# Kernel tuning notes

Measured on AMD Instinct MI355X. Metric: run time of the kernel, lower is better.

Reference implementation:

```python
import jax, jax.numpy as jnp
import numpy as np

B, L, D, H = 4, 1024, 1024, 16
HS = D // H
BLOCK = 1024
EPS = 1e-5


def setup_inputs() -> dict:
    key = jax.random.key(0)
    ks = jax.random.split(key, 12)
    s = 0.02
    return {
        "x": jax.random.normal(ks[0], (B, L, D), jnp.float32),
        "ln1_w": jnp.ones((D,), jnp.float32),
        "ln1_b": jnp.zeros((D,), jnp.float32),
        "Wqkv": jax.random.normal(ks[1], (D, 3 * D), jnp.float32) * s,
        "bqkv": jnp.zeros((3 * D,), jnp.float32),
        "Wproj": jax.random.normal(ks[2], (D, D), jnp.float32) * s,
        "bproj": jnp.zeros((D,), jnp.float32),
        "Er": jax.random.normal(ks[3], (BLOCK, HS), jnp.float32) * s,
        "ln2_w": jnp.ones((D,), jnp.float32),
        "ln2_b": jnp.zeros((D,), jnp.float32),
        "Wfc": jax.random.normal(ks[4], (D, 4 * D), jnp.float32) * s,
        "bfc": jnp.zeros((4 * D,), jnp.float32),
        "Wfc2": jax.random.normal(ks[5], (4 * D, D), jnp.float32) * s,
        "bfc2": jnp.zeros((D,), jnp.float32),
    }


def _layernorm(x, w, b):
    mu = jnp.mean(x, axis=-1, keepdims=True)
    var = jnp.mean(jnp.square(x - mu), axis=-1, keepdims=True)
    return (x - mu) * jax.lax.rsqrt(var + EPS) * w + b


def _skew(QEr):
    # Music-Transformer skew: pad one zero column on the left of last dim,
    # reshape (B,H,L,L+1) -> (B,H,L+1,L), drop first row.
    b, h, l, _ = QEr.shape
    padded = jnp.pad(QEr, ((0, 0), (0, 0), (0, 0), (1, 0)))
    return padded.reshape(b, h, l + 1, l)[:, :, 1:, :]


def _block(x, ln1_w, ln1_b, Wqkv, bqkv, Wproj, bproj, Er,
           ln2_w, ln2_b, Wfc, bfc, Wfc2, bfc2):
    b, l, d = x.shape
    # --- attention on ln_1(x) ---
    h = _layernorm(x, ln1_w, ln1_b)
    qkv = h @ Wqkv + bqkv                      # (B, L, 3D)
    q, k, v = jnp.split(qkv, 3, axis=-1)
    q = q.reshape(b, l, H, HS).transpose(0, 2, 1, 3)  # (B,H,L,hs)
    k = k.reshape(b, l, H, HS).transpose(0, 2, 1, 3)
    v = v.reshape(b, l, H, HS).transpose(0, 2, 1, 3)

    start = BLOCK - l
    Er_t = Er[start:, :].T                     # (hs, L)
    QEr = jnp.einsum('bhld,dm->bhlm', q, Er_t)  # (B,H,L,L)
    Srel = _skew(QEr)

    QKt = jnp.einsum('bhld,bhmd->bhlm', q, k)  # (B,H,L,L)
    scale = 1.0 / jnp.sqrt(jnp.asarray(HS, x.dtype))
    att = (QKt + Srel) * scale
    causal = jnp.tril(jnp.ones((l, l), bool))
    att = jnp.where(causal, att, jnp.asarray(-jnp.inf, att.dtype))
    att = jax.nn.softmax(att, axis=-1)
    y = jnp.einsum('bhlm,bhmd->bhld', att, v)  # (B,H,L,hs)
    y = y.transpose(0, 2, 1, 3).reshape(b, l, d)
    a = y @ Wproj + bproj

    x = x + a
    # --- MLP on ln_2(x) ---
    h2 = _layernorm(x, ln2_w, ln2_b)
    m = jax.nn.gelu(h2 @ Wfc + bfc, approximate=False) @ Wfc2 + bfc2
    return x + m


def reference(x, ln1_w, ln1_b, Wqkv, bqkv, Wproj, bproj, Er,
              ln2_w, ln2_b, Wfc, bfc, Wfc2, bfc2):
    return _block(x, ln1_w, ln1_b, Wqkv, bqkv, Wproj, bproj, Er,
                  ln2_w, ln2_b, Wfc, bfc, Wfc2, bfc2)
```

## Files before the change

### kernel.cpp

```cpp
#include <hip/hip_runtime.h>
#include <hip/hip_bf16.h>
#include <math.h>

typedef __attribute__((ext_vector_type(8))) __bf16 bf16x8;
typedef __attribute__((ext_vector_type(4))) float f32x4;

#define LL 1024
#define DD 1024
#define HH 16

#define GLOAD16(g, l)                                              \
  __builtin_amdgcn_global_load_lds(                                \
      (const __attribute__((address_space(1))) void*)(g),          \
      (__attribute__((address_space(3))) void*)(l), 16, 0, 0)

#define FENCE asm volatile("" ::: "memory")
#define SCHEDB __builtin_amdgcn_sched_barrier(0)
#define BARRIER do { FENCE; __builtin_amdgcn_s_barrier(); FENCE; } while (0)

__global__ __launch_bounds__(256) void prep_weights(const float* __restrict__ Wqkv,
                                                    const float* __restrict__ Wproj,
                                                    const float* __restrict__ Wfc,
                                                    const float* __restrict__ Wfc2,
                                                    const float* __restrict__ Er,
                                                    __hip_bfloat16* __restrict__ Wqkvt,
                                                    __hip_bfloat16* __restrict__ Wprojt,
                                                    __hip_bfloat16* __restrict__ Wfct,
                                                    __hip_bfloat16* __restrict__ Wfc2t,
                                                    __hip_bfloat16* __restrict__ Erb) {
  int bid = blockIdx.x;
  int tx = threadIdx.x;
  if (bid >= 12288) {
    int i = (bid - 12288) * 256 + tx;
    float4 v = *(const float4*)&Er[(size_t)i * 4];
    __hip_bfloat16 o[4];
    o[0] = __float2bfloat16(v.x); o[1] = __float2bfloat16(v.y);
    o[2] = __float2bfloat16(v.z); o[3] = __float2bfloat16(v.w);
    *(uint2*)&Erb[(size_t)i * 4] = *(const uint2*)o;
    return;
  }
  const float* W; __hip_bfloat16* Wt; int R, C, local;
  if (bid < 3072)      { W = Wqkv;  Wt = Wqkvt;  R = 1024; C = 3072; local = bid; }
  else if (bid < 4096) { W = Wproj; Wt = Wprojt; R = 1024; C = 1024; local = bid - 3072; }
  else if (bid < 8192) { W = Wfc;   Wt = Wfct;   R = 1024; C = 4096; local = bid - 4096; }
  else                 { W = Wfc2;  Wt = Wfc2t;  R = 4096; C = 1024; local = bid - 8192; }
  int nbx = C / 32;
  int r0 = (local / nbx) * 32, c0 = (local % nbx) * 32;
  __shared__ float tile[32][33];
  int r = tx >> 3, c4 = (tx & 7) * 4;
  float4 v = *(const float4*)&W[(size_t)(r0 + r) * C + c0 + c4];
  tile[r][c4 + 0] = v.x; tile[r][c4 + 1] = v.y;
  tile[r][c4 + 2] = v.z; tile[r][c4 + 3] = v.w;
  __syncthreads();
  int c = tx >> 3, r4 = (tx & 7) * 4;
  __hip_bfloat16 o[4];
#pragma unroll
  for (int j = 0; j < 4; ++j) o[j] = __float2bfloat16(tile[r4 + j][c]);
  *(uint2*)&Wt[(size_t)(c0 + c) * R + r0 + r4] = *(const uint2*)o;
}

__global__ __launch_bounds__(256) void ln_kernel(const float* __restrict__ X,
                                                 const float* __restrict__ w,
                                                 const float* __restrict__ b,
                                                 __hip_bfloat16* __restrict__ out) {
  int row = blockIdx.x;
  int tid = threadIdx.x;
  const float* xr = X + (size_t)row * DD;
  float4 v = *(const float4*)&xr[tid * 4];
  float s = v.x + v.y + v.z + v.w;
  float s2 = v.x * v.x + v.y * v.y + v.z * v.z + v.w * v.w;
#pragma unroll
  for (int m = 1; m < 64; m <<= 1) {
    s += __shfl_xor(s, m);
    s2 += __shfl_xor(s2, m);
  }
  __shared__ float ps[4], ps2[4];
  int wv_ = tid >> 6, lane = tid & 63;
  if (lane == 0) { ps[wv_] = s; ps2[wv_] = s2; }
  __syncthreads();
  float ts = ps[0] + ps[1] + ps[2] + ps[3];
  float ts2 = ps2[0] + ps2[1] + ps2[2] + ps2[3];
  float mu = ts * (1.0f / DD);
  float var = ts2 * (1.0f / DD) - mu * mu;
  float rs = rsqrtf(var + 1e-5f);
  float4 wv = *(const float4*)&w[tid * 4];
  float4 bv = *(const float4*)&b[tid * 4];
  __hip_bfloat16 o[4];
  o[0] = __float2bfloat16((v.x - mu) * rs * wv.x + bv.x);
  o[1] = __float2bfloat16((v.y - mu) * rs * wv.y + bv.y);
  o[2] = __float2bfloat16((v.z - mu) * rs * wv.z + bv.z);
  o[3] = __float2bfloat16((v.w - mu) * rs * wv.w + bv.w);
  *(uint2*)&out[(size_t)row * DD + tid * 4] = *(const uint2*)o;
}

template <int EPI>
__global__ __launch_bounds__(256, 4) void gemm128sq(const __hip_bfloat16* __restrict__ A,
                                                    const __hip_bfloat16* __restrict__ Bt,
                                                    const float* __restrict__ bias,
                                                    const float* __restrict__ resid,
                                                    void* __restrict__ Cout,
                                                    int M, int N, int K) {
  __shared__ __hip_bfloat16 Ab[2][128][32];
  __shared__ __hip_bfloat16 Bb[2][128][32];
  const int tid = threadIdx.x, lane = tid & 63, w = tid >> 6;
  const int wm = w >> 1, wn = w & 1;

  int nbx = gridDim.x, nwg = nbx * gridDim.y;
  int orig = blockIdx.y * nbx + blockIdx.x;
  int cpx = nwg >> 3;
  int wgid = (orig & 7) * cpx + (orig >> 3);
  int bm0 = (wgid / nbx) * 128, bn0 = (wgid % nbx) * 128;

  const int fr = lane & 15, kq = lane >> 4;
  const int sg = ((lane & 3) ^ ((lane >> 3) & 3)) * 8;
  const int srw = lane >> 2;

  auto stageA = [&](int c, int g, int k0) {
    int u = w * 2 + g;
    const __hip_bfloat16* src = A + (size_t)(bm0 + u * 16 + srw) * K + k0 + sg;
    GLOAD16(src, (char*)Ab + c * 8192 + u * 1024);
  };
  auto stageB = [&](int c, int g, int k0) {
    int u = w * 2 + g;
    const __hip_bfloat16* src = Bt + (size_t)(bn0 + u * 16 + srw) * K + k0 + sg;
    GLOAD16(src, (char*)Bb + c * 8192 + u * 1024);
  };
  const int swz = ((kq ^ ((fr >> 1) & 3)) << 4);
  auto ldA = [&](int c, int r) -> bf16x8 {
    return *(const bf16x8*)((const char*)Ab + c * 8192 + r * 64 + swz);
  };
  auto ldB = [&](int c, int r) -> bf16x8 {
    return *(const bf16x8*)((const char*)Bb + c * 8192 + r * 64 + swz);
  };

  f32x4 acc[4][4] = {};
  bf16x8 a[4], b[4];

  const int nt = K >> 5;
  stageA(0, 0, 0);  stageA(0, 1, 0);  stageB(0, 0, 0);  stageB(0, 1, 0);
  stageA(1, 0, 32); stageA(1, 1, 32); stageB(1, 0, 32); stageB(1, 1, 32);
  asm volatile("s_waitcnt vmcnt(4)" ::: "memory");
  BARRIER;

  for (int t = 0; t < nt; ++t) {
    const int cur = t & 1;
#pragma unroll
    for (int mf = 0; mf < 4; ++mf) a[mf] = ldA(cur, wm * 64 + mf * 16 + fr);
#pragma unroll
    for (int nf = 0; nf < 4; ++nf) b[nf] = ldB(cur, wn * 64 + nf * 16 + fr);
    __builtin_amdgcn_s_setprio(1);
#pragma unroll
    for (int mf = 0; mf < 4; ++mf)
#pragma unroll
      for (int nf = 0; nf < 4; ++nf)
        acc[mf][nf] = __builtin_amdgcn_mfma_f32_16x16x32_bf16(a[mf], b[nf], acc[mf][nf], 0, 0, 0);
    __builtin_amdgcn_s_setprio(0);
    BARRIER;
    if (t + 2 < nt) {
      int kn = (t + 2) * 32;
      stageA(cur, 0, kn); stageA(cur, 1, kn); stageB(cur, 0, kn); stageB(cur, 1, kn);
      asm volatile("s_waitcnt vmcnt(4)" ::: "memory");
    } else if (t + 1 < nt) {
      asm volatile("s_waitcnt vmcnt(0)" ::: "memory");
    }
    BARRIER;
  }

#pragma unroll
  for (int nf = 0; nf < 4; ++nf) {
    int col = bn0 + wn * 64 + nf * 16 + fr;
    float bsv = bias[col];
#pragma unroll
    for (int mf = 0; mf < 4; ++mf) {
      int rowb = bm0 + wm * 64 + mf * 16 + kq * 4;
#pragma unroll
      for (int j = 0; j < 4; ++j) {
        int row = rowb + j;
        float v = acc[mf][nf][j] + bsv;
        if (EPI == 1) v = 0.5f * v * (1.0f + erff(v * 0.7071067811865476f));
        if (EPI == 2) {
          ((float*)Cout)[(size_t)row * N + col] = v + resid[(size_t)row * N + col];
        } else {
          ((__hip_bfloat16*)Cout)[(size_t)row * N + col] = __float2bfloat16(v);
        }
      }
    }
  }
}

template <int EPI>
__global__ __launch_bounds__(512, 4) void gemm128x64w8(const __hip_bfloat16* __restrict__ A,
                                                       const __hip_bfloat16* __restrict__ Bt,
                                                       const float* __restrict__ bias,
                                                       const float* __restrict__ resid,
                                                       void* __restrict__ Cout,
                                                       int M, int N, int K) {
  __shared__ __hip_bfloat16 Ab[3][128][64];
  __shared__ __hip_bfloat16 Bb[3][64][64];
  const int tid = threadIdx.x, lane = tid & 63, w = tid >> 6;
  const int wm = w >> 1, wn = w & 1;

  int nbx = gridDim.x, nwg = nbx * gridDim.y;
  int orig = blockIdx.y * nbx + blockIdx.x;
  int cpx = nwg >> 3;
  int wgid = (orig & 7) * cpx + (orig >> 3);
  int bm0 = (wgid / nbx) * 128, bn0 = (wgid % nbx) * 64;

  const int fr = lane & 15, kq = lane >> 4;
  const int srw = lane >> 3;
  const int sg = ((lane & 7) ^ (lane >> 3)) * 8;

  auto stageA = [&](int c, int j, int k0) {
    int u = 2 * w + j;
    const __hip_bfloat16* src = A + (size_t)(bm0 + u * 8 + srw) * K + k0 + sg;
    GLOAD16(src, (char*)Ab + c * 16384 + u * 1024);
  };
  auto stageB = [&](int c, int k0) {
    const __hip_bfloat16* src = Bt + (size_t)(bn0 + w * 8 + srw) * K + k0 + sg;
    GLOAD16(src, (char*)Bb + c * 8192 + w * 1024);
  };
  auto ldA = [&](int c, int r, int ks) -> bf16x8 {
    int byte = r * 128 + ((ks * 64 + kq * 16) ^ ((r & 7) << 4));
    return *(const bf16x8*)((const char*)Ab + c * 16384 + byte);
  };
  auto ldB = [&](int c, int r, int ks) -> bf16x8 {
    int byte = r * 128 + ((ks * 64 + kq * 16) ^ ((r & 7) << 4));
    return *(const bf16x8*)((const char*)Bb + c * 8192 + byte);
  };

  f32x4 acc[2][2] = {};
  bf16x8 a[2][2], b[2][2];

  const int nt = K >> 6;
#pragma unroll
  for (int tt = 0; tt < 2; ++tt) {
    stageA(tt, 0, tt * 64); stageA(tt, 1, tt * 64); stageB(tt, tt * 64);
  }
  asm volatile("s_waitcnt vmcnt(3)" ::: "memory");
  BARRIER;

  int cur = 0, nxt = 2;
  for (int t = 0; t < nt; ++t) {
#pragma unroll
    for (int mf = 0; mf < 2; ++mf)
#pragma unroll
      for (int ks = 0; ks < 2; ++ks)
        a[mf][ks] = ldA(cur, wm * 32 + mf * 16 + fr, ks);
#pragma unroll
    for (int nf = 0; nf < 2; ++nf)
#pragma unroll
      for (int ks = 0; ks < 2; ++ks)
        b[nf][ks] = ldB(cur, wn * 32 + nf * 16 + fr, ks);
    if (t + 2 < nt) {
      stageA(nxt, 0, (t + 2) * 64); stageA(nxt, 1, (t + 2) * 64); stageB(nxt, (t + 2) * 64);
    }
    __builtin_amdgcn_s_setprio(1);
#pragma unroll
    for (int mf = 0; mf < 2; ++mf)
#pragma unroll
      for (int nf = 0; nf < 2; ++nf)
#pragma unroll
        for (int ks = 0; ks < 2; ++ks)
          acc[mf][nf] = __builtin_amdgcn_mfma_f32_16x16x32_bf16(
              a[mf][ks], b[nf][ks], acc[mf][nf], 0, 0, 0);
    __builtin_amdgcn_s_setprio(0);
    if (t <= nt - 3)      { asm volatile("s_waitcnt vmcnt(3)" ::: "memory"); }
    else if (t == nt - 2) { asm volatile("s_waitcnt vmcnt(0)" ::: "memory"); }
    BARRIER;
    cur = (cur == 2) ? 0 : cur + 1;
    nxt = (nxt == 2) ? 0 : nxt + 1;
  }

#pragma unroll
  for (int nf = 0; nf < 2; ++nf) {
    int col = bn0 + wn * 32 + nf * 16 + fr;
    float bsv = bias[col];
#pragma unroll
    for (int mf = 0; mf < 2; ++mf) {
      int rowb = bm0 + wm * 32 + mf * 16 + kq * 4;
#pragma unroll
      for (int j = 0; j < 4; ++j) {
        int row = rowb + j;
        float v = acc[mf][nf][j] + bsv;
        if (EPI == 1) v = 0.5f * v * (1.0f + erff(v * 0.7071067811865476f));
        if (EPI == 2) {
          ((float*)Cout)[(size_t)row * N + col] = v + resid[(size_t)row * N + col];
        } else {
          ((__hip_bfloat16*)Cout)[(size_t)row * N + col] = __float2bfloat16(v);
        }
      }
    }
  }
}

__global__ __launch_bounds__(256) void attn_mfma(const __hip_bfloat16* __restrict__ qkv,
                                                 const __hip_bfloat16* __restrict__ Erb,
                                                 __hip_bfloat16* __restrict__ Y) {
  __shared__ __hip_bfloat16 k_s[64][72];
  __shared__ __hip_bfloat16 er_s[64][72];
  __shared__ __hip_bfloat16 p_s[4][16][72];
  __shared__ __hip_bfloat16 g_s[4][16][132];
  __shared__ __hip_bfloat16 vt_s[64 * 64];

  int bid = blockIdx.x;
  int qi = 15 - (bid >> 6);
  int head = bid & 63;
  int h = head & 15, b = head >> 4;
  int l0 = qi * 64;
  int tid = threadIdx.x, lane = tid & 63, w = tid >> 6;
  const int fr = lane & 15, kq = lane >> 4;

  const __hip_bfloat16* base = qkv + (size_t)b * (LL * 3072) + h * 64;

  bf16x8 qf[2];
  {
    const __hip_bfloat16* q0 = base + (size_t)(l0 + 16 * w + fr) * 3072 + kq * 8;
    qf[0] = *(const bf16x8*)q0;
    qf[1] = *(const bf16x8*)(q0 + 32);
  }

  const int ksr = tid >> 2, ksd = (tid & 3) * 16;
  const __hip_bfloat16* ksrc = base + 1024 + (size_t)ksr * 3072 + ksd;
  const int vc = (tid >> 3) * 2, vd0 = (tid & 7) * 8;
  const __hip_bfloat16* vsrc = base + 2048 + (size_t)vc * 3072 + vd0;
  const int err = tid >> 2, erc = (tid & 3) * 16;

  uint4 kst0, kst1, vst0, vst1;
  uint4 ers0, ers1;
  uint4 ec10, ec11;

  {
    kst0 = *(const uint4*)ksrc; kst1 = *(const uint4*)(ksrc + 8);
    vst0 = *(const uint4*)vsrc; vst1 = *(const uint4*)(vsrc + 3072);
    int m0 = min(max(960 - l0 + err, 0), 1023);
    const __hip_bfloat16* ep0 = Erb + (size_t)m0 * 64 + erc;
    ers0 = *(const uint4*)ep0; ers1 = *(const uint4*)(ep0 + 8);
    if (qi > 0) {
      int m1 = min(max(960 - l0 + 64 + err, 0), 1023);
      const __hip_bfloat16* ep1 = Erb + (size_t)m1 * 64 + erc;
      ec10 = *(const uint4*)ep1; ec11 = *(const uint4*)(ep1 + 8);
    }
  }

  f32x4 oacc[4] = {};
  float m_run[4], s_run[4];
#pragma unroll
  for (int j = 0; j < 4; ++j) { m_run[j] = -1e30f; s_run[j] = 0.f; }

  auto gchunk = [&](int hf) {
#pragma unroll
    for (int g = 0; g < 4; ++g) {
      int cc = 16 * g + fr, kc = kq * 8;
      bf16x8 e0 = *(const bf16x8*)&er_s[cc][kc];
      bf16x8 e1 = *(const bf16x8*)&er_s[cc][kc + 32];
      f32x4 gacc = {};
      gacc = __builtin_amdgcn_mfma_f32_16x16x32_bf16(qf[0], e0, gacc, 0, 0, 0);
      gacc = __builtin_amdgcn_mfma_f32_16x16x32_bf16(qf[1], e1, gacc, 0, 0, 0);
#pragma unroll
      for (int j = 0; j < 4; ++j)
        g_s[w][kq * 4 + j][hf * 64 + 16 * g + fr] = __float2bfloat16(gacc[j]);
    }
  };

  for (int t = 0; t <= qi; ++t) {
    __syncthreads();
    *(uint4*)&k_s[ksr][ksd] = kst0;
    *(uint4*)&k_s[ksr][ksd + 8] = kst1;
    {
      const uint16_t* h0 = (const uint16_t*)&vst0;
      const uint16_t* h1 = (const uint16_t*)&vst1;
#pragma unroll
      for (int j = 0; j < 8; ++j) {
        int d = vd0 + j;
        uint32_t pk = (uint32_t)h0[j] | ((uint32_t)h1[j] << 16);
        uint32_t byte = ((uint32_t)d << 7) + 2u * (uint32_t)vc;
        byte ^= (uint32_t)(((d & 7) ^ (d >> 3)) << 4);
        *(uint32_t*)((char*)vt_s + byte) = pk;
      }
    }
    if (t == 0 || t < qi) {
      *(uint4*)&er_s[err][erc]     = ers0;
      *(uint4*)&er_s[err][erc + 8] = ers1;
    }
    __syncthreads();
    if (t < qi) {
      int c0n = (t + 1) * 64;
      const __hip_bfloat16* kp = ksrc + (size_t)c0n * 3072;
      kst0 = *(const uint4*)kp; kst1 = *(const uint4*)(kp + 8);
      const __hip_bfloat16* vp = vsrc + (size_t)c0n * 3072;
      vst0 = *(const uint4*)vp; vst1 = *(const uint4*)(vp + 3072);
      if (t + 1 < qi) {
        int m = min(960 - l0 + (t + 2) * 64 + err, 1023);
        const __hip_bfloat16* ep = Erb + (size_t)m * 64 + erc;
        ers0 = *(const uint4*)ep; ers1 = *(const uint4*)(ep + 8);
      }
    }
    SCHEDB;

    f32x4 sacc[4] = {};
#pragma unroll
    for (int f = 0; f < 4; ++f) {
      int cc = 16 * f + fr, kc = kq * 8;
      bf16x8 k0 = *(const bf16x8*)&k_s[cc][kc];
      bf16x8 k1 = *(const bf16x8*)&k_s[cc][kc + 32];
      sacc[f] = __builtin_amdgcn_mfma_f32_16x16x32_bf16(qf[0], k0, sacc[f], 0, 0, 0);
      sacc[f] = __builtin_amdgcn_mfma_f32_16x16x32_bf16(qf[1], k1, sacc[f], 0, 0, 0);
    }
    if (t == 0) {
      gchunk(0);
      if (qi > 0) {
        __syncthreads();
        *(uint4*)&er_s[err][erc]     = ec10;
        *(uint4*)&er_s[err][erc + 8] = ec11;
        __syncthreads();
        gchunk(1);
      }
    } else if (t < qi) {
      gchunk((t + 1) & 1);
    }

    float sv[4][4];
#pragma unroll
    for (int f = 0; f < 4; ++f) {
#pragma unroll
      for (int j = 0; j < 4; ++j) {
        int r = kq * 4 + j;
        int c = 16 * f + fr;
        int jj = c - (16 * w + r) + 63;
        float g = __bfloat162float(g_s[w][r][(t * 64 + jj) & 127]);
        float val = (sacc[f][j] + g) * 0.125f;
        if (t == qi && c > 16 * w + r) val = -1e30f;
        sv[f][j] = val;
      }
    }
    float tm[4];
#pragma unroll
    for (int j = 0; j < 4; ++j) {
      float m_ = fmaxf(fmaxf(sv[0][j], sv[1][j]), fmaxf(sv[2][j], sv[3][j]));
      m_ = fmaxf(m_, __shfl_xor(m_, 1));
      m_ = fmaxf(m_, __shfl_xor(m_, 2));
      m_ = fmaxf(m_, __shfl_xor(m_, 4));
      m_ = fmaxf(m_, __shfl_xor(m_, 8));
      tm[j] = m_;
    }
    bool need = (tm[0] > m_run[0] + 8.f) || (tm[1] > m_run[1] + 8.f) ||
                (tm[2] > m_run[2] + 8.f) || (tm[3] > m_run[3] + 8.f);
    float alpha[4];
    if (need) {
#pragma unroll
      for (int j = 0; j < 4; ++j) {
        float nm = fmaxf(m_run[j], tm[j]);
        alpha[j] = __expf(m_run[j] - nm);
        m_run[j] = nm;
      }
    }
#pragma unroll
    for (int f = 0; f < 4; ++f)
#pragma unroll
      for (int j = 0; j < 4; ++j)
        sv[f][j] = __expf(sv[f][j] - m_run[j]);
#pragma unroll
    for (int j = 0; j < 4; ++j) {
      float ps = sv[0][j] + sv[1][j] + sv[2][j] + sv[3][j];
      ps += __shfl_xor(ps, 1); ps += __shfl_xor(ps, 2);
      ps += __shfl_xor(ps, 4); ps += __shfl_xor(ps, 8);
      s_run[j] = (need ? s_run[j] * alpha[j] : s_run[j]) + ps;
    }
    if (need) {
#pragma unroll
      for (int f = 0; f < 4; ++f)
#pragma unroll
        for (int j = 0; j < 4; ++j)
          oacc[f][j] *= alpha[j];
    }
#pragma unroll
    for (int f = 0; f < 4; ++f)
#pragma unroll
      for (int j = 0; j < 4; ++j)
        p_s[w][kq * 4 + j][16 * f + fr] = __float2bfloat16(sv[f][j]);
#pragma unroll
    for (int kk = 0; kk < 2; ++kk) {
      bf16x8 pf = *(const bf16x8*)&p_s[w][fr][kq * 8 + 32 * kk];
#pragma unroll
      for (int f = 0; f < 4; ++f) {
        int d = 16 * f + fr;
        int cc = kq * 8 + 32 * kk;
        uint32_t byte = ((uint32_t)d << 7) + 2u * (uint32_t)cc;
        byte ^= (uint32_t)(((d & 7) ^ (d >> 3)) << 4);
        bf16x8 vf = *(const bf16x8*)((char*)vt_s + byte);
        oacc[f] = __builtin_amdgcn_mfma_f32_16x16x32_bf16(pf, vf, oacc[f], 0, 0, 0);
      }
    }
  }

#pragma unroll
  for (int f = 0; f < 4; ++f)
#pragma unroll
    for (int j = 0; j < 4; ++j) {
      int r = 16 * w + kq * 4 + j;
      int d = 16 * f + fr;
      float o = oacc[f][j] / s_run[j];
      Y[(size_t)(b * LL + l0 + r) * DD + h * 64 + d] = __float2bfloat16(o);
    }
}

extern "C" void kernel_launch(void* const* d_in, const int* in_sizes, int n_in,
                              void* d_out, int out_size, void* d_ws, size_t ws_size,
                              hipStream_t stream) {
  (void)in_sizes; (void)n_in; (void)out_size; (void)ws_size;
  const float* x     = (const float*)d_in[0];
  const float* ln1w  = (const float*)d_in[1];
  const float* ln1b  = (const float*)d_in[2];
  const float* Wqkv  = (const float*)d_in[3];
  const float* bqkv  = (const float*)d_in[4];
  const float* Wproj = (const float*)d_in[5];
  const float* bproj = (const float*)d_in[6];
  const float* Er    = (const float*)d_in[7];
  const float* ln2w  = (const float*)d_in[8];
  const float* ln2b  = (const float*)d_in[9];
  const float* Wfc   = (const float*)d_in[10];
  const float* bfc   = (const float*)d_in[11];
  const float* Wfc2  = (const float*)d_in[12];
  const float* bfc2  = (const float*)d_in[13];
  float* out = (float*)d_out;

  char* ws = (char*)d_ws;
  const size_t MB = 1ull << 20;
  __hip_bfloat16* h1    = (__hip_bfloat16*)(ws + 0);
  __hip_bfloat16* qkvb  = (__hip_bfloat16*)(ws + 8 * MB);
  __hip_bfloat16* mbuf  = (__hip_bfloat16*)(ws + 0);
  __hip_bfloat16* yb    = (__hip_bfloat16*)(ws + 32 * MB);
  __hip_bfloat16* h2    = (__hip_bfloat16*)(ws + 32 * MB);
  float*          x2    = (float*)(ws + 40 * MB);
  __hip_bfloat16* Wqkvt = (__hip_bfloat16*)(ws + 56 * MB);
  __hip_bfloat16* Erb   = (__hip_bfloat16*)(ws + 62 * MB);
  __hip_bfloat16* Wprojt= (__hip_bfloat16*)(ws + 63 * MB);
  __hip_bfloat16* Wfct  = (__hip_bfloat16*)(ws + 66 * MB);
  __hip_bfloat16* Wfc2t = (__hip_bfloat16*)(ws + 75 * MB);

  dim3 blk(256);

  prep_weights<<<dim3(12352), blk, 0, stream>>>(Wqkv, Wproj, Wfc, Wfc2, Er,
                                                Wqkvt, Wprojt, Wfct, Wfc2t, Erb);

  ln_kernel<<<4096, blk, 0, stream>>>(x, ln1w, ln1b, h1);

  gemm128sq<0><<<dim3(3072 / 128, 4096 / 128), blk, 0, stream>>>(
      h1, Wqkvt, bqkv, nullptr, qkvb, 4096, 3072, 1024);

  attn_mfma<<<dim3(1024), blk, 0, stream>>>(qkvb, Erb, yb);

  gemm128x64w8<2><<<dim3(1024 / 64, 4096 / 128), dim3(512), 0, stream>>>(
      yb, Wprojt, bproj, x, x2, 4096, 1024, 1024);

  ln_kernel<<<4096, blk, 0, stream>>>(x2, ln2w, ln2b, h2);

  gemm128sq<1><<<dim3(4096 / 128, 4096 / 128), blk, 0, stream>>>(
      h2, Wfct, bfc, nullptr, mbuf, 4096, 4096, 1024);

  gemm128x64w8<2><<<dim3(1024 / 64, 4096 / 128), dim3(512), 0, stream>>>(
      mbuf, Wfc2t, bfc2, x2, out, 4096, 1024, 4096);
}
```

Before: 223.9 us.

## Replace LDS-staged GEMM with direct global-to-register double-buffered loads

The 128x128 GEMM used for QKV and FC1 no longer stages A and B tiles through shared memory. Each wave now loads its MFMA fragments straight from global memory into registers, double-buffered across k-steps, and all barriers are gone. The workgroup-to-tile remapping is also changed to a new XCD-aware grouping. The aim is to remove LDS traffic and sync overhead, at the cost of redundant global/L2 reads across waves and higher register pressure (launch bounds lowered to 3).

```diff
diff --git a/kernel.cpp b/kernel.cpp
--- a/kernel.cpp
+++ b/kernel.cpp
@@ -94,60 +94,38 @@
 }
 
 template <int EPI>
-__global__ __launch_bounds__(256, 4) void gemm128sq(const __hip_bfloat16* __restrict__ A,
-                                                    const __hip_bfloat16* __restrict__ Bt,
-                                                    const float* __restrict__ bias,
-                                                    const float* __restrict__ resid,
-                                                    void* __restrict__ Cout,
-                                                    int M, int N, int K) {
-  __shared__ __hip_bfloat16 Ab[2][128][32];
-  __shared__ __hip_bfloat16 Bb[2][128][32];
+__global__ __launch_bounds__(256, 3) void gemm128d(const __hip_bfloat16* __restrict__ A,
+                                                   const __hip_bfloat16* __restrict__ Bt,
+                                                   const float* __restrict__ bias,
+                                                   const float* __restrict__ resid,
+                                                   void* __restrict__ Cout,
+                                                   int M, int N, int K) {
   const int tid = threadIdx.x, lane = tid & 63, w = tid >> 6;
   const int wm = w >> 1, wn = w & 1;
 
   int nbx = gridDim.x, nwg = nbx * gridDim.y;
   int orig = blockIdx.y * nbx + blockIdx.x;
-  int cpx = nwg >> 3;
-  int wgid = (orig & 7) * cpx + (orig >> 3);
-  int bm0 = (wgid / nbx) * 128, bn0 = (wgid % nbx) * 128;
+  int cpx = nwg >> 3, CC = cpx >> 3;
+  int x = orig & 7, kk = orig >> 3;
+  int row = ((x >> 1) << 3) + (kk & 7);
+  int col = (x & 1) * CC + (kk >> 3);
+  int bm0 = row * 128, bn0 = col * 128;
 
   const int fr = lane & 15, kq = lane >> 4;
-  const int sg = ((lane & 3) ^ ((lane >> 3) & 3)) * 8;
-  const int srw = lane >> 2;
-
-  auto stageA = [&](int c, int g, int k0) {
-    int u = w * 2 + g;
-    const __hip_bfloat16* src = A + (size_t)(bm0 + u * 16 + srw) * K + k0 + sg;
-    GLOAD16(src, (char*)Ab + c * 8192 + u * 1024);
-  };
-  auto stageB = [&](int c, int g, int k0) {
-    int u = w * 2 + g;
-    const __hip_bfloat16* src = Bt + (size_t)(bn0 + u * 16 + srw) * K + k0 + sg;
-    GLOAD16(src, (char*)Bb + c * 8192 + u * 1024);
-  };
-  const int swz = ((kq ^ ((fr >> 1) & 3)) << 4);
-  auto ldA = [&](int c, int r) -> bf16x8 {
-    return *(const bf16x8*)((const char*)Ab + c * 8192 + r * 64 + swz);
-  };
-  auto ldB = [&](int c, int r) -> bf16x8 {
-    return *(const bf16x8*)((const char*)Bb + c * 8192 + r * 64 + swz);
-  };
+
+  const __hip_bfloat16* ap[4];
+  const __hip_bfloat16* bp[4];
+#pragma unroll
+  for (int mf = 0; mf < 4; ++mf)
+    ap[mf] = A + (size_t)(bm0 + wm * 64 + mf * 16 + fr) * K + kq * 8;
+#pragma unroll
+  for (int nf = 0; nf < 4; ++nf)
+    bp[nf] = Bt + (size_t)(bn0 + wn * 64 + nf * 16 + fr) * K + kq * 8;
 
   f32x4 acc[4][4] = {};
-  bf16x8 a[4], b[4];
-
-  const int nt = K >> 5;
-  stageA(0, 0, 0);  stageA(0, 1, 0);  stageB(0, 0, 0);  stageB(0, 1, 0);
-  stageA(1, 0, 32); stageA(1, 1, 32); stageB(1, 0, 32); stageB(1, 1, 32);
-  asm volatile("s_waitcnt vmcnt(4)" ::: "memory");
-  BARRIER;
-
-  for (int t = 0; t < nt; ++t) {
-    const int cur = t & 1;
-#pragma unroll
-    for (int mf = 0; mf < 4; ++mf) a[mf] = ldA(cur, wm * 64 + mf * 16 + fr);
-#pragma unroll
-    for (int nf = 0; nf < 4; ++nf) b[nf] = ldB(cur, wn * 64 + nf * 16 + fr);
+  bf16x8 a0[4], b0[4], a1[4], b1[4];
+
+  auto mmq = [&](bf16x8* a, bf16x8* b) {
     __builtin_amdgcn_s_setprio(1);
 #pragma unroll
     for (int mf = 0; mf < 4; ++mf)
@@ -155,33 +133,45 @@
       for (int nf = 0; nf < 4; ++nf)
         acc[mf][nf] = __builtin_amdgcn_mfma_f32_16x16x32_bf16(a[mf], b[nf], acc[mf][nf], 0, 0, 0);
     __builtin_amdgcn_s_setprio(0);
-    BARRIER;
+  };
+
+  const int nt = K >> 5;
+#pragma unroll
+  for (int mf = 0; mf < 4; ++mf) a0[mf] = *(const bf16x8*)ap[mf];
+#pragma unroll
+  for (int nf = 0; nf < 4; ++nf) b0[nf] = *(const bf16x8*)bp[nf];
+
+  for (int t = 0; t < nt; t += 2) {
+#pragma unroll
+    for (int mf = 0; mf < 4; ++mf) a1[mf] = *(const bf16x8*)(ap[mf] + (t + 1) * 32);
+#pragma unroll
+    for (int nf = 0; nf < 4; ++nf) b1[nf] = *(const bf16x8*)(bp[nf] + (t + 1) * 32);
+    mmq(a0, b0);
     if (t + 2 < nt) {
-      int kn = (t + 2) * 32;
-      stageA(cur, 0, kn); stageA(cur, 1, kn); stageB(cur, 0, kn); stageB(cur, 1, kn);
-      asm volatile("s_waitcnt vmcnt(4)" ::: "memory");
-    } else if (t + 1 < nt) {
-      asm volatile("s_waitcnt vmcnt(0)" ::: "memory");
-    }
-    BARRIER;
+#pragma unroll
+      for (int mf = 0; mf < 4; ++mf) a0[mf] = *(const bf16x8*)(ap[mf] + (t + 2) * 32);
+#pragma unroll
+      for (int nf = 0; nf < 4; ++nf) b0[nf] = *(const bf16x8*)(bp[nf] + (t + 2) * 32);
+    }
+    mmq(a1, b1);
   }
 
 #pragma unroll
   for (int nf = 0; nf < 4; ++nf) {
-    int col = bn0 + wn * 64 + nf * 16 + fr;
-    float bsv = bias[col];
+    int colo = bn0 + wn * 64 + nf * 16 + fr;
+    float bsv = bias[colo];
 #pragma unroll
     for (int mf = 0; mf < 4; ++mf) {
       int rowb = bm0 + wm * 64 + mf * 16 + kq * 4;
 #pragma unroll
       for (int j = 0; j < 4; ++j) {
-        int row = rowb + j;
+        int rr = rowb + j;
         float v = acc[mf][nf][j] + bsv;
         if (EPI == 1) v = 0.5f * v * (1.0f + erff(v * 0.7071067811865476f));
         if (EPI == 2) {
-          ((float*)Cout)[(size_t)row * N + col] = v + resid[(size_t)row * N + col];
+          ((float*)Cout)[(size_t)rr * N + colo] = v + resid[(size_t)rr * N + colo];
         } else {
-          ((__hip_bfloat16*)Cout)[(size_t)row * N + col] = __float2bfloat16(v);
+          ((__hip_bfloat16*)Cout)[(size_t)rr * N + colo] = __float2bfloat16(v);
         }
       }
     }
@@ -545,7 +535,7 @@
 
   ln_kernel<<<4096, blk, 0, stream>>>(x, ln1w, ln1b, h1);
 
-  gemm128sq<0><<<dim3(3072 / 128, 4096 / 128), blk, 0, stream>>>(
+  gemm128d<0><<<dim3(3072 / 128, 4096 / 128), blk, 0, stream>>>(
       h1, Wqkvt, bqkv, nullptr, qkvb, 4096, 3072, 1024);
 
   attn_mfma<<<dim3(1024), blk, 0, stream>>>(qkvb, Erb, yb);
@@ -555,7 +545,7 @@
 
   ln_kernel<<<4096, blk, 0, stream>>>(x2, ln2w, ln2b, h2);
 
-  gemm128sq<1><<<dim3(4096 / 128, 4096 / 128), blk, 0, stream>>>(
+  gemm128d<1><<<dim3(4096 / 128, 4096 / 128), blk, 0, stream>>>(
       h2, Wfct, bfc, nullptr, mbuf, 4096, 4096, 1024);
 
   gemm128x64w8<2><<<dim3(1024 / 64, 4096 / 128), dim3(512), 0, stream>>>(
```

Result: slower. 345.9 us (+54.5%).
